# Kernel optimization log

Measured on AMD Instinct MI355X. Metric: run time of the kernel, lower is better.

Reference implementation:

```python
import jax, jax.numpy as jnp
import numpy as np

B, S = 128, 2048
INPUT_DIM, CTX_DIM = 512, 512


def setup_inputs() -> dict:
    key = jax.random.key(0)
    ks = jax.random.split(key, 9)
    s_in = 1.0 / np.sqrt(INPUT_DIM)
    s_ctx = 1.0 / np.sqrt(CTX_DIM)
    s_out = 1.0 / np.sqrt(INPUT_DIM + CTX_DIM)
    inp = {
        "input": jax.random.normal(ks[0], (B, INPUT_DIM), jnp.float32),
        "context": jax.random.normal(ks[1], (B, S, CTX_DIM), jnp.float32),
        "context_mask": jax.random.randint(ks[2], (B, S), 0, 2) > 0,  # True = masked
        # params (torch Linear stores W as [out,in]; we store [in,out] for x @ W)
        "W_in": jax.random.uniform(ks[3], (INPUT_DIM, CTX_DIM), jnp.float32, -s_in, s_in),
        "b_in": jax.random.uniform(ks[4], (CTX_DIM,), jnp.float32, -s_in, s_in),
        "W_ctx": jax.random.uniform(ks[5], (CTX_DIM, CTX_DIM), jnp.float32, -s_ctx, s_ctx),
        "b_ctx": jax.random.uniform(ks[6], (CTX_DIM,), jnp.float32, -s_ctx, s_ctx),
        "w_score": jax.random.uniform(ks[7], (CTX_DIM,), jnp.float32, -s_ctx, s_ctx),
        "W_out": jax.random.uniform(ks[8], (INPUT_DIM + CTX_DIM, INPUT_DIM), jnp.float32, -s_out, s_out),
        "b_out": jax.random.uniform(jax.random.fold_in(key, 99), (INPUT_DIM,), jnp.float32, -s_out, s_out),
    }
    # ensure at least one unmasked position per row (avoid all -inf softmax)
    inp["context_mask"] = inp["context_mask"].at[:, 0].set(False)
    return inp


def reference(input, context, context_mask, W_in, b_in, W_ctx, b_ctx, w_score, W_out, b_out):
    # input: [B, Di], context: [B, S, Dc]
    q = input @ W_in + b_in                              # [B, Dc]
    k = jnp.einsum("bsd,de->bse", context, W_ctx) + b_ctx  # [B, S, Dc]
    # additive score: v^T tanh(q + k)
    scores = jnp.einsum("bsd,d->bs", jnp.tanh(q[:, None, :] + k), w_score)  # [B, S]
    scores = jnp.where(context_mask, -jnp.inf, scores)
    attn = jax.nn.softmax(scores, axis=-1)               # [B, S]
    ctx_vec = jnp.einsum("bs,bsd->bd", attn, context)    # [B, Dc]
    x = jnp.tanh(jnp.concatenate([ctx_vec, input], axis=1) @ W_out + b_out)  # [B, Di]
    return (x, attn)
```

## Files before the change

### kernel.cpp

```cpp
#include <hip/hip_runtime.h>
#include <hip/hip_bf16.h>
#include <math.h>

#define B_  128
#define S_  2048
#define DI  512
#define DC  512

typedef __attribute__((ext_vector_type(8))) __bf16 bf16x8;
typedef __attribute__((ext_vector_type(4))) float  f32x4;
typedef __attribute__((ext_vector_type(8))) unsigned short us8;

__device__ __forceinline__ float fast_tanh(float x) {
    float e = __expf(2.f * x);
    return 1.f - 2.f * __builtin_amdgcn_rcpf(e + 1.f);
}

__device__ __forceinline__ unsigned short f2bf(float f) {
    unsigned int u = __float_as_uint(f);
    u += 0x7FFF + ((u >> 16) & 1);
    return (unsigned short)(u >> 16);
}

__device__ __forceinline__ float bf2f(unsigned int lo16) {
    return __uint_as_float(lo16 << 16);
}

__global__ __launch_bounds__(256) void qb_kernel(
    const float* __restrict__ input, const float* __restrict__ W_in,
    const float* __restrict__ b_in, const float* __restrict__ b_ctx,
    float* __restrict__ qb)
{
    __shared__ float sIn[DI];
    int b = blockIdx.x, t = threadIdx.x;
    for (int i = t; i < DI; i += 256) sIn[i] = input[b * DI + i];
    __syncthreads();
    int e0 = t * 2;
    float a0 = b_in[e0] + b_ctx[e0];
    float a1 = b_in[e0 + 1] + b_ctx[e0 + 1];
    for (int d = 0; d < DI; ++d) {
        float v = sIn[d];
        const float* w = W_in + (size_t)d * DC + e0;
        a0 += v * w[0];
        a1 += v * w[1];
    }
    qb[b * DC + e0] = a0;
    qb[b * DC + e0 + 1] = a1;
}

__global__ __launch_bounds__(256) void wt_kernel(
    const float* __restrict__ W_ctx, unsigned short* __restrict__ WtF)
{
    int tid = blockIdx.x * 256 + threadIdx.x;
    int s   = tid >> 11;
    int rem = tid & 2047;
    int g   = rem >> 6;
    int l   = rem & 63;
    int c   = g * 16 + (l & 15);
    int k0  = s * 32 + (l >> 4) * 8;
    us8 w;
    #pragma unroll
    for (int j = 0; j < 8; ++j)
        w[j] = f2bf(W_ctx[(size_t)(k0 + j) * DC + c]);
    *(us8*)(WtF + (size_t)tid * 8) = w;
}

__global__ __launch_bounds__(256, 2) void score_kernel(
    const float* __restrict__ ctx,
    const unsigned short* __restrict__ WtF,
    const float* __restrict__ qb,
    const float* __restrict__ wsc,
    const int* __restrict__ mask,
    float* __restrict__ scores_ws,
    float* __restrict__ pv_ws,
    float* __restrict__ ml_ws)
{
    __shared__ __align__(16) unsigned short ctxs[64 * 512];
    __shared__ float sred[4][64];
    __shared__ float sp[64];

    const int t = threadIdx.x;
    const int row0 = blockIdx.x * 64;
    const int bidx = row0 >> 11;
    const int lane = t & 63;
    const int wc = t >> 6;
    const int lr = lane & 15, half = lane >> 4;

    #pragma unroll
    for (int i = 0; i < 16; ++i) {
        int u = i * 256 + t;
        int r = u >> 6, kg = u & 63;
        const float4* src = (const float4*)(ctx + (size_t)(row0 + r) * DC + kg * 8);
        float4 va = src[0], vb = src[1];
        us8 w;
        w[0] = f2bf(va.x); w[1] = f2bf(va.y); w[2] = f2bf(va.z); w[3] = f2bf(va.w);
        w[4] = f2bf(vb.x); w[5] = f2bf(vb.y); w[6] = f2bf(vb.z); w[7] = f2bf(vb.w);
        *(us8*)((char*)ctxs + ((r * 1024 + kg * 16) ^ ((r & 7) << 4))) = w;
    }
    __syncthreads();

    f32x4 acc[4][8] = {};
    #pragma unroll 2
    for (int s = 0; s < 16; ++s) {
        bf16x8 bfr[8];
        const us8* wsrc = (const us8*)(WtF + ((size_t)(s * 32 + wc * 8) * 64 + lane) * 8);
        #pragma unroll
        for (int fn = 0; fn < 8; ++fn)
            bfr[fn] = *(const bf16x8*)(wsrc + fn * 64);
        bf16x8 af[4];
        #pragma unroll
        for (int fm = 0; fm < 4; ++fm) {
            int r = fm * 16 + lr;
            af[fm] = *(const bf16x8*)((const char*)ctxs +
                        ((r * 1024 + s * 64 + half * 16) ^ ((r & 7) << 4)));
        }
        #pragma unroll
        for (int fm = 0; fm < 4; ++fm)
            #pragma unroll
            for (int fn = 0; fn < 8; ++fn)
                acc[fm][fn] = __builtin_amdgcn_mfma_f32_16x16x32_bf16(
                    af[fm], bfr[fn], acc[fm][fn], 0, 0, 0);
    }

    float wv[8], qv[8];
    #pragma unroll
    for (int fn = 0; fn < 8; ++fn) {
        int j = wc * 128 + fn * 16 + lr;
        wv[fn] = wsc[j];
        qv[fn] = qb[bidx * DC + j];
    }
    #pragma unroll
    for (int fm = 0; fm < 4; ++fm) {
        #pragma unroll
        for (int reg = 0; reg < 4; ++reg) {
            float ssum = 0.f;
            #pragma unroll
            for (int fn = 0; fn < 8; ++fn)
                ssum += wv[fn] * fast_tanh(qv[fn] + acc[fm][fn][reg]);
            #pragma unroll
            for (int m = 8; m >= 1; m >>= 1)
                ssum += __shfl_xor(ssum, m, 64);
            if (lr == 0)
                sred[wc][fm * 16 + half * 4 + reg] = ssum;
        }
    }
    __syncthreads();

    if (t < 64) {
        float sc = sred[0][t] + sred[1][t] + sred[2][t] + sred[3][t];
        if (mask[row0 + t] != 0) sc = -1e30f;
        scores_ws[row0 + t] = sc;
        float mx = sc;
        #pragma unroll
        for (int m = 32; m >= 1; m >>= 1) mx = fmaxf(mx, __shfl_xor(mx, m, 64));
        float pe = __expf(sc - mx);
        sp[t] = pe;
        float ls = pe;
        #pragma unroll
        for (int m = 32; m >= 1; m >>= 1) ls += __shfl_xor(ls, m, 64);
        if (t == 0) {
            ml_ws[blockIdx.x * 2]     = mx;
            ml_ws[blockIdx.x * 2 + 1] = ls;
        }
    }
    __syncthreads();

    int d0 = t * 2;
    float a0 = 0.f, a1 = 0.f;
    #pragma unroll 8
    for (int s = 0; s < 64; ++s) {
        float w = sp[s];
        unsigned int u = *(const unsigned int*)
            ((const char*)ctxs + ((s * 1024 + d0 * 2) ^ ((s & 7) << 4)));
        a0 += w * bf2f(u & 0xffffu);
        a1 += w * bf2f(u >> 16);
    }
    pv_ws[(size_t)blockIdx.x * 512 + d0]     = a0;
    pv_ws[(size_t)blockIdx.x * 512 + d0 + 1] = a1;
}

__global__ __launch_bounds__(256) void combine_kernel(
    const float* __restrict__ pv, const float* __restrict__ ml,
    const float* __restrict__ scores,
    float* __restrict__ ctxv, float* __restrict__ attn)
{
    int b = blockIdx.x, t = threadIdx.x;
    __shared__ float sm[32], sl[32], sw[32];
    if (t < 32) {
        sm[t] = ml[(b * 32 + t) * 2];
        sl[t] = ml[(b * 32 + t) * 2 + 1];
    }
    __syncthreads();
    float mstar = -1e30f;
    #pragma unroll
    for (int i = 0; i < 32; ++i) mstar = fmaxf(mstar, sm[i]);
    if (t < 32) sw[t] = __expf(sm[t] - mstar);
    __syncthreads();
    float L = 0.f;
    #pragma unroll
    for (int i = 0; i < 32; ++i) L += sw[i] * sl[i];
    float invL = 1.f / L;

    int d0 = t * 2;
    float c0 = 0.f, c1 = 0.f;
    #pragma unroll
    for (int i = 0; i < 32; ++i) {
        float w = sw[i];
        const float2 v = *(const float2*)(pv + (size_t)(b * 32 + i) * 512 + d0);
        c0 += w * v.x; c1 += w * v.y;
    }
    ctxv[b * DC + d0]     = c0 * invL;
    ctxv[b * DC + d0 + 1] = c1 * invL;

    for (int s = t; s < S_; s += 256)
        attn[(size_t)b * S_ + s] = __expf(scores[(size_t)b * S_ + s] - mstar) * invL;
}

__global__ __launch_bounds__(256) void out_kernel(
    const float* __restrict__ ctxv, const float* __restrict__ input,
    const float* __restrict__ W_out, const float* __restrict__ b_out,
    float* __restrict__ x)
{
    __shared__ float sc[DC + DI];
    int b = blockIdx.x, t = threadIdx.x;
    for (int i = t; i < DC; i += 256) sc[i] = ctxv[b * DC + i];
    for (int i = t; i < DI; i += 256) sc[DC + i] = input[b * DI + i];
    __syncthreads();
    int e0 = t * 2;
    float a0 = b_out[e0], a1 = b_out[e0 + 1];
    for (int d = 0; d < DC + DI; ++d) {
        float v = sc[d];
        const float* w = W_out + (size_t)d * DI + e0;
        a0 += v * w[0];
        a1 += v * w[1];
    }
    x[b * DI + e0] = fast_tanh(a0);
    x[b * DI + e0 + 1] = fast_tanh(a1);
}

extern "C" void kernel_launch(void* const* d_in, const int* in_sizes, int n_in,
                              void* d_out, int out_size, void* d_ws, size_t ws_size,
                              hipStream_t stream) {
    const float* input = (const float*)d_in[0];
    const float* ctx   = (const float*)d_in[1];
    const int*   mask  = (const int*)d_in[2];
    const float* W_in  = (const float*)d_in[3];
    const float* b_in  = (const float*)d_in[4];
    const float* W_ctx = (const float*)d_in[5];
    const float* b_ctx = (const float*)d_in[6];
    const float* wsc   = (const float*)d_in[7];
    const float* W_out = (const float*)d_in[8];
    const float* b_out = (const float*)d_in[9];

    float* x_out = (float*)d_out;
    float* attn  = (float*)d_out + B_ * DI;

    const int NBLK = (B_ * S_) / 64;

    char* ws = (char*)d_ws;
    float* qb = (float*)ws;                    ws += (size_t)B_ * DC * 4;
    unsigned short* WtF = (unsigned short*)ws; ws += (size_t)DC * DC * 2;
    float* scores_ws = (float*)ws;             ws += (size_t)B_ * S_ * 4;
    float* pv_ws = (float*)ws;                 ws += (size_t)NBLK * 512 * 4;
    float* ml_ws = (float*)ws;                 ws += (size_t)NBLK * 2 * 4;
    float* ctxv = (float*)ws;                  ws += (size_t)B_ * DC * 4;

    qb_kernel<<<B_, 256, 0, stream>>>(input, W_in, b_in, b_ctx, qb);
    wt_kernel<<<(16 * 32 * 64) / 256, 256, 0, stream>>>(W_ctx, WtF);
    score_kernel<<<NBLK, 256, 0, stream>>>(ctx, WtF, qb, wsc, mask,
                                           scores_ws, pv_ws, ml_ws);
    combine_kernel<<<B_, 256, 0, stream>>>(pv_ws, ml_ws, scores_ws, ctxv, attn);
    out_kernel<<<B_, 256, 0, stream>>>(ctxv, input, W_out, b_out, x_out);
}
```

Before: 317.8 us.

## Use 512-thread score blocks with 8 waves splitting output columns

The score kernel moves from 4 waves to 8 waves per block, each wave covering 64 output columns instead of 128. This halves the accumulator registers per wave, and launch bounds ask for more resident waves, so more memory latency can be hidden. The bf16 conversion in the staging loop switches to the packed __float22bfloat162_rn intrinsic. The P·V pass now has each thread handle one column with 16-bit LDS reads, and the score reduction sums 8 partials instead of 4.

```diff
diff --git a/kernel.cpp b/kernel.cpp
--- a/kernel.cpp
+++ b/kernel.cpp
@@ -20,6 +20,12 @@
     unsigned int u = __float_as_uint(f);
     u += 0x7FFF + ((u >> 16) & 1);
     return (unsigned short)(u >> 16);
+}
+
+__device__ __forceinline__ unsigned int pk2(float a, float b) {
+    union { __hip_bfloat162 h; unsigned int u; } c;
+    c.h = __float22bfloat162_rn(make_float2(a, b));
+    return c.u;
 }
 
 __device__ __forceinline__ float bf2f(unsigned int lo16) {
@@ -65,7 +71,7 @@
     *(us8*)(WtF + (size_t)tid * 8) = w;
 }
 
-__global__ __launch_bounds__(256, 2) void score_kernel(
+__global__ __launch_bounds__(512, 4) void score_kernel(
     const float* __restrict__ ctx,
     const unsigned short* __restrict__ WtF,
     const float* __restrict__ qb,
@@ -76,36 +82,37 @@
     float* __restrict__ ml_ws)
 {
     __shared__ __align__(16) unsigned short ctxs[64 * 512];
-    __shared__ float sred[4][64];
+    __shared__ float sred[8][64];
     __shared__ float sp[64];
 
     const int t = threadIdx.x;
     const int row0 = blockIdx.x * 64;
     const int bidx = row0 >> 11;
     const int lane = t & 63;
-    const int wc = t >> 6;
+    const int w = t >> 6;
     const int lr = lane & 15, half = lane >> 4;
 
     #pragma unroll
-    for (int i = 0; i < 16; ++i) {
-        int u = i * 256 + t;
+    for (int i = 0; i < 8; ++i) {
+        int u = i * 512 + t;
         int r = u >> 6, kg = u & 63;
         const float4* src = (const float4*)(ctx + (size_t)(row0 + r) * DC + kg * 8);
         float4 va = src[0], vb = src[1];
-        us8 w;
-        w[0] = f2bf(va.x); w[1] = f2bf(va.y); w[2] = f2bf(va.z); w[3] = f2bf(va.w);
-        w[4] = f2bf(vb.x); w[5] = f2bf(vb.y); w[6] = f2bf(vb.z); w[7] = f2bf(vb.w);
-        *(us8*)((char*)ctxs + ((r * 1024 + kg * 16) ^ ((r & 7) << 4))) = w;
-    }
-    __syncthreads();
-
-    f32x4 acc[4][8] = {};
+        unsigned int p0 = pk2(va.x, va.y), p1 = pk2(va.z, va.w);
+        unsigned int p2 = pk2(vb.x, vb.y), p3 = pk2(vb.z, vb.w);
+        uint4 pk = {p0, p1, p2, p3};
+        *(uint4*)((char*)ctxs + ((r * 1024 + kg * 16) ^ ((r & 7) << 4))) = pk;
+    }
+    __syncthreads();
+
+    f32x4 acc[4][4] = {};
     #pragma unroll 2
     for (int s = 0; s < 16; ++s) {
-        bf16x8 bfr[8];
-        const us8* wsrc = (const us8*)(WtF + ((size_t)(s * 32 + wc * 8) * 64 + lane) * 8);
-        #pragma unroll
-        for (int fn = 0; fn < 8; ++fn)
+        bf16x8 bfr[4];
+        const us8* wsrc = (const us8*)(WtF +
+            (((size_t)s * 32 + w * 4) * 64 + lane) * 8);
+        #pragma unroll
+        for (int fn = 0; fn < 4; ++fn)
             bfr[fn] = *(const bf16x8*)(wsrc + fn * 64);
         bf16x8 af[4];
         #pragma unroll
@@ -117,15 +124,15 @@
         #pragma unroll
         for (int fm = 0; fm < 4; ++fm)
             #pragma unroll
-            for (int fn = 0; fn < 8; ++fn)
+            for (int fn = 0; fn < 4; ++fn)
                 acc[fm][fn] = __builtin_amdgcn_mfma_f32_16x16x32_bf16(
                     af[fm], bfr[fn], acc[fm][fn], 0, 0, 0);
     }
 
-    float wv[8], qv[8];
-    #pragma unroll
-    for (int fn = 0; fn < 8; ++fn) {
-        int j = wc * 128 + fn * 16 + lr;
+    float wv[4], qv[4];
+    #pragma unroll
+    for (int fn = 0; fn < 4; ++fn) {
+        int j = w * 64 + fn * 16 + lr;
         wv[fn] = wsc[j];
         qv[fn] = qb[bidx * DC + j];
     }
@@ -135,19 +142,20 @@
         for (int reg = 0; reg < 4; ++reg) {
             float ssum = 0.f;
             #pragma unroll
-            for (int fn = 0; fn < 8; ++fn)
+            for (int fn = 0; fn < 4; ++fn)
                 ssum += wv[fn] * fast_tanh(qv[fn] + acc[fm][fn][reg]);
             #pragma unroll
             for (int m = 8; m >= 1; m >>= 1)
                 ssum += __shfl_xor(ssum, m, 64);
             if (lr == 0)
-                sred[wc][fm * 16 + half * 4 + reg] = ssum;
+                sred[w][fm * 16 + half * 4 + reg] = ssum;
         }
     }
     __syncthreads();
 
     if (t < 64) {
-        float sc = sred[0][t] + sred[1][t] + sred[2][t] + sred[3][t];
+        float sc = sred[0][t] + sred[1][t] + sred[2][t] + sred[3][t]
+                 + sred[4][t] + sred[5][t] + sred[6][t] + sred[7][t];
         if (mask[row0 + t] != 0) sc = -1e30f;
         scores_ws[row0 + t] = sc;
         float mx = sc;
@@ -165,18 +173,14 @@
     }
     __syncthreads();
 
-    int d0 = t * 2;
-    float a0 = 0.f, a1 = 0.f;
+    float a0 = 0.f;
     #pragma unroll 8
     for (int s = 0; s < 64; ++s) {
-        float w = sp[s];
-        unsigned int u = *(const unsigned int*)
-            ((const char*)ctxs + ((s * 1024 + d0 * 2) ^ ((s & 7) << 4)));
-        a0 += w * bf2f(u & 0xffffu);
-        a1 += w * bf2f(u >> 16);
-    }
-    pv_ws[(size_t)blockIdx.x * 512 + d0]     = a0;
-    pv_ws[(size_t)blockIdx.x * 512 + d0 + 1] = a1;
+        unsigned int u = *(const unsigned short*)
+            ((const char*)ctxs + ((s * 1024 + t * 2) ^ ((s & 7) << 4)));
+        a0 += sp[s] * bf2f(u);
+    }
+    pv_ws[(size_t)blockIdx.x * 512 + t] = a0;
 }
 
 __global__ __launch_bounds__(256) void combine_kernel(
@@ -267,7 +271,7 @@
 
     qb_kernel<<<B_, 256, 0, stream>>>(input, W_in, b_in, b_ctx, qb);
     wt_kernel<<<(16 * 32 * 64) / 256, 256, 0, stream>>>(W_ctx, WtF);
-    score_kernel<<<NBLK, 256, 0, stream>>>(ctx, WtF, qb, wsc, mask,
+    score_kernel<<<NBLK, 512, 0, stream>>>(ctx, WtF, qb, wsc, mask,
                                            scores_ws, pv_ws, ml_ws);
     combine_kernel<<<B_, 256, 0, stream>>>(pv_ws, ml_ws, scores_ws, ctxv, attn);
     out_kernel<<<B_, 256, 0, stream>>>(ctxv, input, W_out, b_out, x_out);
```

New measurement: 284.9 us. 1.12x faster.
